# Performance work log

Measured on AMD Instinct MI355X. Metric: run time of the kernel, lower is better.

## Reference

```python
import jax, jax.numpy as jnp
import numpy as np

M, B, N, D, DFF, DCOND = 8, 8, 2048, 512, 2048, 512


def setup_inputs() -> dict:
    key = jax.random.key(0)
    ks = jax.random.split(key, 8)
    s = 0.02  # weight init scale
    return {
        "x": jax.random.normal(ks[0], (B, N, D), dtype=jnp.float32),
        "cond": jax.random.normal(ks[1], (B, DCOND), dtype=jnp.float32),
        "route": jax.random.randint(ks[2], (B,), 0, M, dtype=jnp.int64),
        "W_cond": jax.random.normal(ks[3], (M, DCOND, 2 * D), dtype=jnp.float32) * s,
        "b_cond": jnp.zeros((M, 2 * D), dtype=jnp.float32),
        "W1": jax.random.normal(ks[4], (M, D, DFF), dtype=jnp.float32) * s,
        "b1": jnp.zeros((M, DFF), dtype=jnp.float32),
        "W2": jax.random.normal(ks[5], (M, DFF, D), dtype=jnp.float32) * s,
        "b2": jnp.zeros((M, D), dtype=jnp.float32),
    }


def reference(x, cond, route, W_cond, b_cond, W1, b1, W2, b2):
    # --- all branches computed densely (faithful to the torch module) ---
    # cond modulation per branch: [M, B, 2D]
    mod = jnp.einsum('bc,mcd->mbd', cond, W_cond) + b_cond[:, None, :]
    scale, shift = jnp.split(mod, 2, axis=-1)            # each [M, B, D]
    # FiLM modulate tokens: [M, B, N, D]
    x_mod = x[None] * (1.0 + scale[:, :, None, :]) + shift[:, :, None, :]
    # MLP per branch
    h = jax.nn.gelu(jnp.einsum('mbnd,mdf->mbnf', x_mod, W1) + b1[:, None, None, :])
    stacked = jnp.einsum('mbnf,mfd->mbnd', h, W2) + b2[:, None, None, :]  # [M,B,N,D]
    # --- one-hot select (torch.einsum('mbnd,bm->bnd', stacked, one_hot)) ---
    one_hot = jax.nn.one_hot(route, M, dtype=stacked.dtype)  # [B, M]
    return jnp.einsum('mbnd,bm->bnd', stacked, one_hot)
```

## Files before the change

kernel.cpp:

```cpp
#include <hip/hip_runtime.h>
#include <hip/hip_bf16.h>
#include <cstdint>
#include <cstddef>

#define NEXP   8
#define BATCH  8
#define NTOK   2048
#define DDIM   512
#define DFFDIM 2048
#define DCOND  512

typedef float  f32x4  __attribute__((ext_vector_type(4)));
typedef __bf16 bf16x8 __attribute__((ext_vector_type(8)));

using as1_cvoid = __attribute__((address_space(1))) const void;
using as3_void  = __attribute__((address_space(3))) void;

__device__ __forceinline__ void async_copy16(const void* g, void* l) {
  __builtin_amdgcn_global_load_lds((as1_cvoid*)g, (as3_void*)l, 16, 0, 0);
}

__device__ __forceinline__ unsigned short f2bf_bits(float f) {
  __hip_bfloat16 h = __float2bfloat16(f);
  return *reinterpret_cast<unsigned short*>(&h);
}

__device__ __forceinline__ float gelu_fast(float v) {
  float y = v * fmaf(0.0713548162726f, v * v, 1.5957691216057f);
  float e = exp2f(-1.44269504089f * y);
  return v * __builtin_amdgcn_rcpf(1.0f + e);
}

__global__ void mod_kernel(const float* __restrict__ cond,
                           const int* __restrict__ route,
                           const float* __restrict__ W_cond,
                           const float* __restrict__ b_cond,
                           float* __restrict__ ss) {
  const int b = blockIdx.y;
  const int m = route[b];
  const int tj = threadIdx.x & 63;
  const int cq = threadIdx.x >> 6;
  const int j = blockIdx.x * 64 + tj;
  const float* wc = W_cond + (size_t)m * DCOND * (2 * DDIM);
  const float* cb = cond + (size_t)b * DCOND;
  float acc = 0.f;
#pragma unroll 4
  for (int c = cq * 128; c < cq * 128 + 128; ++c)
    acc += cb[c] * wc[(size_t)c * (2 * DDIM) + j];
  __shared__ float red[4][64];
  red[cq][tj] = acc;
  __syncthreads();
  if (cq == 0) {
    float v = red[0][tj] + red[1][tj] + red[2][tj] + red[3][tj];
    ss[(size_t)b * (2 * DDIM) + j] = v + b_cond[(size_t)m * (2 * DDIM) + j];
  }
}

__global__ void film_kernel(const float* __restrict__ x,
                            const float* __restrict__ ss,
                            __hip_bfloat16* __restrict__ xmod) {
  const size_t idx = (size_t)blockIdx.x * blockDim.x + threadIdx.x;
  const int d4 = (int)(idx & (DDIM / 4 - 1));
  const int b  = (int)(idx >> 18);
  const float4 xv = reinterpret_cast<const float4*>(x)[idx];
  const float4 sc = reinterpret_cast<const float4*>(ss + (size_t)b * 1024)[d4];
  const float4 sh = reinterpret_cast<const float4*>(ss + (size_t)b * 1024 + DDIM)[d4];
  float r0 = xv.x * (1.f + sc.x) + sh.x;
  float r1 = xv.y * (1.f + sc.y) + sh.y;
  float r2 = xv.z * (1.f + sc.z) + sh.z;
  float r3 = xv.w * (1.f + sc.w) + sh.w;
  ushort4 ov;
  ov.x = f2bf_bits(r0); ov.y = f2bf_bits(r1);
  ov.z = f2bf_bits(r2); ov.w = f2bf_bits(r3);
  reinterpret_cast<ushort4*>(xmod)[idx] = ov;
}

__global__ void transpose_cvt(const float* __restrict__ in,
                              __hip_bfloat16* __restrict__ outp,
                              int L, int R,
                              const int* __restrict__ route) {
  const int mi = blockIdx.z;
  bool used = false;
#pragma unroll
  for (int b = 0; b < BATCH; ++b) used |= (route[b] == mi);
  if (!used) return;

  __shared__ float tile[32][33];
  const float* inm = in + (size_t)mi * L * R;
  __hip_bfloat16* outm = outp + (size_t)mi * L * R;
  const int r0 = blockIdx.x * 32, l0 = blockIdx.y * 32;
  const int tx = threadIdx.x, ty = threadIdx.y;
#pragma unroll
  for (int i = 0; i < 32; i += 8)
    tile[ty + i][tx] = inm[(size_t)(l0 + ty + i) * R + r0 + tx];
  __syncthreads();
#pragma unroll
  for (int i = 0; i < 32; i += 8)
    outm[(size_t)(r0 + ty + i) * L + l0 + tx] = __float2bfloat16(tile[tx][ty + i]);
}

template <int EPI>
__global__ __launch_bounds__(256, 2) void gemm_db2(
    const __hip_bfloat16* __restrict__ Abase,
    const __hip_bfloat16* __restrict__ Btbase,
    const float* __restrict__ biasbase,
    void* __restrict__ outbase,
    const int* __restrict__ route,
    int Mdim, int Ndim, int Kdim, int tilesX) {
  const int bid  = blockIdx.x;
  const int b    = bid & 7;
  const int tile = bid >> 3;
  const int bx   = tile % tilesX;
  const int by   = tile / tilesX;
  const int m = route[b];
  const __hip_bfloat16* A  = Abase  + (size_t)b * Mdim * Kdim;
  const __hip_bfloat16* Bt = Btbase + (size_t)m * Ndim * Kdim;
  const float* bias = biasbase + (size_t)m * Ndim;
  const int r0 = bx * 128;
  const int n0 = by * 128;

  __shared__ alignas(16) __hip_bfloat16 As[2][128 * 64];
  __shared__ alignas(16) __hip_bfloat16 Bs[2][128 * 64];

  const int t = threadIdx.x;
  const int w = t >> 6, l = t & 63;
  const int wr = w >> 1, wc = w & 1;

  const int srow = t >> 3;
  const int scol = (t & 7) ^ ((t >> 3) & 7);

#define STAGE(s_, k0)                                                         \
  { _Pragma("unroll")                                                         \
    for (int i = 0; i < 4; ++i)                                               \
      async_copy16(A + (size_t)(r0 + i * 32 + srow) * Kdim + (k0) + scol * 8, \
                   &As[s_][(i * 256 + t) * 8]);                               \
    _Pragma("unroll")                                                         \
    for (int i = 0; i < 4; ++i)                                               \
      async_copy16(Bt + (size_t)(n0 + i * 32 + srow) * Kdim + (k0) + scol * 8,\
                   &Bs[s_][(i * 256 + t) * 8]); }

  const int lrow = l & 15, lq = l >> 4, lx = l & 7;
  f32x4 acc[4][4] = {};
  const int nt = Kdim >> 6;

  STAGE(0, 0)

  for (int kt = 0; kt < nt; ++kt) {
    const int s = kt & 1;
    if (kt + 1 < nt) {
      STAGE(s ^ 1, (kt + 1) * 64)
      asm volatile("s_waitcnt vmcnt(8)" ::: "memory");
    } else {
      asm volatile("s_waitcnt vmcnt(0)" ::: "memory");
    }
    __builtin_amdgcn_s_barrier();
    __builtin_amdgcn_sched_barrier(0);

    const __hip_bfloat16* as_ = As[s];
    const __hip_bfloat16* bs_ = Bs[s];
    bf16x8 af[4][2], bfr[4][2];
#pragma unroll
    for (int mb = 0; mb < 4; ++mb) {
      const int row = wr * 64 + mb * 16 + lrow;
      af[mb][0] = *reinterpret_cast<const bf16x8*>(&as_[(row * 8 + ((0 + lq) ^ lx)) * 8]);
      af[mb][1] = *reinterpret_cast<const bf16x8*>(&as_[(row * 8 + ((4 + lq) ^ lx)) * 8]);
    }
#pragma unroll
    for (int nb = 0; nb < 4; ++nb) {
      const int row = wc * 64 + nb * 16 + lrow;
      bfr[nb][0] = *reinterpret_cast<const bf16x8*>(&bs_[(row * 8 + ((0 + lq) ^ lx)) * 8]);
      bfr[nb][1] = *reinterpret_cast<const bf16x8*>(&bs_[(row * 8 + ((4 + lq) ^ lx)) * 8]);
    }
#pragma unroll
    for (int mb = 0; mb < 4; ++mb)
#pragma unroll
      for (int nb = 0; nb < 4; ++nb) {
        acc[mb][nb] = __builtin_amdgcn_mfma_f32_16x16x32_bf16(
            af[mb][0], bfr[nb][0], acc[mb][nb], 0, 0, 0);
        acc[mb][nb] = __builtin_amdgcn_mfma_f32_16x16x32_bf16(
            af[mb][1], bfr[nb][1], acc[mb][nb], 0, 0, 0);
      }

    __builtin_amdgcn_sched_barrier(0);
    __builtin_amdgcn_s_barrier();
  }
#undef STAGE

  if (EPI == 0) {
    __hip_bfloat16* out = (__hip_bfloat16*)outbase + (size_t)b * Mdim * Ndim;
#pragma unroll
    for (int mb = 0; mb < 4; ++mb) {
      const int row = r0 + wr * 64 + mb * 16 + lq * 4;
#pragma unroll
      for (int nb = 0; nb < 4; ++nb) {
        const int col = n0 + wc * 64 + nb * 16 + lrow;
        const float bv = bias[col];
#pragma unroll
        for (int j = 0; j < 4; ++j) {
          float g = gelu_fast(acc[mb][nb][j] + bv);
          out[(size_t)(row + j) * Ndim + col] = __float2bfloat16(g);
        }
      }
    }
  } else {
    float* out = (float*)outbase + (size_t)b * Mdim * Ndim;
#pragma unroll
    for (int mb = 0; mb < 4; ++mb) {
      const int row = r0 + wr * 64 + mb * 16 + lq * 4;
#pragma unroll
      for (int nb = 0; nb < 4; ++nb) {
        const int col = n0 + wc * 64 + nb * 16 + lrow;
        const float bv = bias[col];
#pragma unroll
        for (int j = 0; j < 4; ++j)
          out[(size_t)(row + j) * Ndim + col] = acc[mb][nb][j] + bv;
      }
    }
  }
}

extern "C" void kernel_launch(void* const* d_in, const int* in_sizes, int n_in,
                              void* d_out, int out_size, void* d_ws, size_t ws_size,
                              hipStream_t stream) {
  const float* x      = (const float*)d_in[0];
  const float* cond   = (const float*)d_in[1];
  const int*   route  = (const int*)d_in[2];
  const float* W_cond = (const float*)d_in[3];
  const float* b_cond = (const float*)d_in[4];
  const float* W1     = (const float*)d_in[5];
  const float* b1     = (const float*)d_in[6];
  const float* W2     = (const float*)d_in[7];
  const float* b2     = (const float*)d_in[8];
  float* out = (float*)d_out;

  const size_t SS_OFF   = 0;
  const size_t XMOD_OFF = 32768;
  const size_t W1T_OFF  = XMOD_OFF + (size_t)BATCH * NTOK * DDIM * 2;
  const size_t W2T_OFF  = W1T_OFF + (size_t)NEXP * DDIM * DFFDIM * 2;
  const size_t H_OFF    = W2T_OFF + (size_t)NEXP * DFFDIM * DDIM * 2;
  const size_t NEED     = H_OFF + (size_t)BATCH * NTOK * DFFDIM * 2;
  if (ws_size < NEED) return;

  char* ws = (char*)d_ws;
  float* ss            = (float*)(ws + SS_OFF);
  __hip_bfloat16* xmod = (__hip_bfloat16*)(ws + XMOD_OFF);
  __hip_bfloat16* w1t  = (__hip_bfloat16*)(ws + W1T_OFF);
  __hip_bfloat16* w2t  = (__hip_bfloat16*)(ws + W2T_OFF);
  __hip_bfloat16* h    = (__hip_bfloat16*)(ws + H_OFF);

  mod_kernel<<<dim3(2 * DDIM / 64, BATCH), 256, 0, stream>>>(cond, route, W_cond, b_cond, ss);

  {
    const size_t groups = (size_t)BATCH * NTOK * DDIM / 4;
    film_kernel<<<(unsigned)(groups / 256), 256, 0, stream>>>(x, ss, xmod);
  }

  transpose_cvt<<<dim3(DFFDIM / 32, DDIM / 32, NEXP), dim3(32, 8), 0, stream>>>(W1, w1t, DDIM, DFFDIM, route);
  transpose_cvt<<<dim3(DDIM / 32, DFFDIM / 32, NEXP), dim3(32, 8), 0, stream>>>(W2, w2t, DFFDIM, DDIM, route);

  gemm_db2<0><<<(NTOK / 128) * (DFFDIM / 128) * BATCH, 256, 0, stream>>>(
      xmod, w1t, b1, h, route, NTOK, DFFDIM, DDIM, NTOK / 128);

  gemm_db2<1><<<(NTOK / 128) * (DDIM / 128) * BATCH, 256, 0, stream>>>(
      h, w2t, b2, out, route, NTOK, DDIM, DFFDIM, NTOK / 128);
}
```

Measured before the change: 137.2 us.

## Load B operand directly into registers in first GEMM, stage only A in LDS

Adds a new GEMM kernel for the first MLP layer. It stages only the A tile (xmod) through LDS with async copies and an XOR swizzle, and loads the B (transposed W1) fragments straight from global memory into registers. Those register fragments are double-buffered across K iterations, with explicit vmcnt waits. The aim is to cut LDS traffic and shared-memory footprint for B. In exchange it costs higher register pressure and uncoalesced, per-wave redundant global reads of weights.

```diff
diff --git a/kernel.cpp b/kernel.cpp
--- a/kernel.cpp
+++ b/kernel.cpp
@@ -99,6 +99,137 @@
     outm[(size_t)(r0 + ty + i) * L + l0 + tx] = __float2bfloat16(tile[tx][ty + i]);
 }
 
+__device__ __forceinline__ void loadB(bf16x8 (&dst)[4][2],
+                                      const __hip_bfloat16* __restrict__ Bt,
+                                      int bn0, int Kdim, int kt,
+                                      int lrow, int lq) {
+#pragma unroll
+  for (int nb = 0; nb < 4; ++nb)
+#pragma unroll
+    for (int kk = 0; kk < 2; ++kk)
+      dst[nb][kk] = *reinterpret_cast<const bf16x8*>(
+          &Bt[(size_t)(bn0 + nb * 16 + lrow) * Kdim + kt * 64 + kk * 32 + lq * 8]);
+}
+
+template <int EPI>
+__global__ __launch_bounds__(256) void gemm_bd(
+    const __hip_bfloat16* __restrict__ Abase,
+    const __hip_bfloat16* __restrict__ Btbase,
+    const float* __restrict__ biasbase,
+    void* __restrict__ outbase,
+    const int* __restrict__ route,
+    int Mdim, int Ndim, int Kdim, int tilesX) {
+  const int bid  = blockIdx.x;
+  const int b    = bid & 7;
+  const int tile = bid >> 3;
+  const int bx   = tile % tilesX;
+  const int by   = tile / tilesX;
+  const int m = route[b];
+  const __hip_bfloat16* A  = Abase  + (size_t)b * Mdim * Kdim;
+  const __hip_bfloat16* Bt = Btbase + (size_t)m * Ndim * Kdim;
+  const float* bias = biasbase + (size_t)m * Ndim;
+  const int r0 = bx * 128;
+  const int n0 = by * 128;
+
+  __shared__ alignas(16) __hip_bfloat16 As[2][128 * 64];
+
+  const int t = threadIdx.x;
+  const int w = t >> 6, l = t & 63;
+  const int wr = w >> 1, wc = w & 1;
+
+  const int srow = t >> 3;
+  const int scol = (t & 7) ^ ((t >> 3) & 7);
+
+#define STAGE_A(s_, k0)                                                       \
+  { _Pragma("unroll")                                                         \
+    for (int i = 0; i < 4; ++i)                                               \
+      async_copy16(A + (size_t)(r0 + i * 32 + srow) * Kdim + (k0) + scol * 8, \
+                   &As[s_][(i * 256 + t) * 8]); }
+
+  const int lrow = l & 15, lq = l >> 4, lx = l & 7;
+  const int bn0 = n0 + wc * 64;
+  f32x4 acc[4][4] = {};
+  const int nt = Kdim >> 6;
+
+  bf16x8 bE[4][2], bO[4][2];
+
+  STAGE_A(0, 0)
+  loadB(bE, Bt, bn0, Kdim, 0, lrow, lq);
+
+#define BODY(t_, s_, bCur, bNxt)                                              \
+  {                                                                           \
+    if ((t_) + 1 < nt) {                                                      \
+      STAGE_A((s_) ^ 1, ((t_) + 1) * 64)                                      \
+      loadB(bNxt, Bt, bn0, Kdim, (t_) + 1, lrow, lq);                         \
+      asm volatile("s_waitcnt vmcnt(12)" ::: "memory");                       \
+    } else {                                                                  \
+      asm volatile("s_waitcnt vmcnt(0)" ::: "memory");                        \
+    }                                                                         \
+    __builtin_amdgcn_s_barrier();                                             \
+    __builtin_amdgcn_sched_barrier(0);                                        \
+    const __hip_bfloat16* as_ = As[s_];                                       \
+    bf16x8 af[4][2];                                                          \
+    _Pragma("unroll")                                                         \
+    for (int mb = 0; mb < 4; ++mb) {                                          \
+      const int row = wr * 64 + mb * 16 + lrow;                               \
+      af[mb][0] = *reinterpret_cast<const bf16x8*>(                           \
+          &as_[(row * 8 + ((0 + lq) ^ lx)) * 8]);                             \
+      af[mb][1] = *reinterpret_cast<const bf16x8*>(                           \
+          &as_[(row * 8 + ((4 + lq) ^ lx)) * 8]);                             \
+    }                                                                         \
+    _Pragma("unroll")                                                         \
+    for (int mb = 0; mb < 4; ++mb)                                            \
+      _Pragma("unroll")                                                       \
+      for (int nb = 0; nb < 4; ++nb) {                                        \
+        acc[mb][nb] = __builtin_amdgcn_mfma_f32_16x16x32_bf16(                \
+            af[mb][0], bCur[nb][0], acc[mb][nb], 0, 0, 0);                    \
+        acc[mb][nb] = __builtin_amdgcn_mfma_f32_16x16x32_bf16(                \
+            af[mb][1], bCur[nb][1], acc[mb][nb], 0, 0, 0);                    \
+      }                                                                       \
+    __builtin_amdgcn_sched_barrier(0);                                        \
+    __builtin_amdgcn_s_barrier();                                             \
+  }
+
+  for (int kt = 0; kt < nt; kt += 2) {
+    BODY(kt,     0, bE, bO)
+    BODY(kt + 1, 1, bO, bE)
+  }
+#undef BODY
+#undef STAGE_A
+
+  if (EPI == 0) {
+    __hip_bfloat16* out = (__hip_bfloat16*)outbase + (size_t)b * Mdim * Ndim;
+#pragma unroll
+    for (int mb = 0; mb < 4; ++mb) {
+      const int row = r0 + wr * 64 + mb * 16 + lq * 4;
+#pragma unroll
+      for (int nb = 0; nb < 4; ++nb) {
+        const int col = n0 + wc * 64 + nb * 16 + lrow;
+        const float bv = bias[col];
+#pragma unroll
+        for (int j = 0; j < 4; ++j) {
+          float g = gelu_fast(acc[mb][nb][j] + bv);
+          out[(size_t)(row + j) * Ndim + col] = __float2bfloat16(g);
+        }
+      }
+    }
+  } else {
+    float* out = (float*)outbase + (size_t)b * Mdim * Ndim;
+#pragma unroll
+    for (int mb = 0; mb < 4; ++mb) {
+      const int row = r0 + wr * 64 + mb * 16 + lq * 4;
+#pragma unroll
+      for (int nb = 0; nb < 4; ++nb) {
+        const int col = n0 + wc * 64 + nb * 16 + lrow;
+        const float bv = bias[col];
+#pragma unroll
+        for (int j = 0; j < 4; ++j)
+          out[(size_t)(row + j) * Ndim + col] = acc[mb][nb][j] + bv;
+      }
+    }
+  }
+}
+
 template <int EPI>
 __global__ __launch_bounds__(256, 2) void gemm_db2(
     const __hip_bfloat16* __restrict__ Abase,
@@ -258,7 +389,7 @@
   transpose_cvt<<<dim3(DFFDIM / 32, DDIM / 32, NEXP), dim3(32, 8), 0, stream>>>(W1, w1t, DDIM, DFFDIM, route);
   transpose_cvt<<<dim3(DDIM / 32, DFFDIM / 32, NEXP), dim3(32, 8), 0, stream>>>(W2, w2t, DFFDIM, DDIM, route);
 
-  gemm_db2<0><<<(NTOK / 128) * (DFFDIM / 128) * BATCH, 256, 0, stream>>>(
+  gemm_bd<0><<<(NTOK / 128) * (DFFDIM / 128) * BATCH, 256, 0, stream>>>(
       xmod, w1t, b1, h, route, NTOK, DFFDIM, DDIM, NTOK / 128);
 
   gemm_db2<1><<<(NTOK / 128) * (DDIM / 128) * BATCH, 256, 0, stream>>>(
```

After: 163.7 us. 1.19x slower.
